# Kernel tuning notes

Measured on AMD Instinct MI355X. Metric: run time of the kernel, lower is better.

The kernel has to match this reference:

```python
import jax, jax.numpy as jnp
import numpy as np

B, IN, OUT, LUT_SIZE = 32, 8192, 16384, 256


def setup_inputs() -> dict:
    key = jax.random.key(0)
    k1, k2, k3 = jax.random.split(key, 3)
    x = jax.random.normal(k1, (B, IN), dtype=jnp.float32)
    # int8 weight codes, stored as indices in [0, 256) into the dequant LUT
    weight_idx = jax.random.randint(k2, (OUT, IN), 0, LUT_SIZE, dtype=jnp.int32)
    # symmetric uniform dequant levels: code c -> (c - 128) * scale
    scale = jnp.float32(0.05 / 128.0)
    lut = (jnp.arange(LUT_SIZE, dtype=jnp.float32) - 128.0) * scale  # [256]
    bias = jax.random.normal(k3, (OUT,), dtype=jnp.float32) * 0.02
    return {"x": x, "lut": lut, "bias": bias, "weight_idx": weight_idx}


def reference(x, lut, bias, weight_idx):
    # LUT dequantization: gather fp32 weight values from the 256-entry table
    W = lut[weight_idx]                      # [OUT, IN] fp32
    # y = x @ W^T + b   (einsum: b=batch tokens, i=in_features, o=out_features)
    return jnp.einsum("bi,oi->bo", x, W) + bias  # [B, OUT]
```

## Files before the change

kernel.cpp:

```cpp
#include <hip/hip_runtime.h>

#define IN_F   8192
#define OUT_F  16384
#define BATCH  32
#define NWAVE  4
#define KSLICE (IN_F / NWAVE)

typedef __attribute__((ext_vector_type(8))) short  bf16x8;
typedef __attribute__((ext_vector_type(4))) float  f32x4;

__device__ __forceinline__ unsigned f2bf(float f) {
    unsigned u = __builtin_bit_cast(unsigned, f);
    return (u + 0x7fffu + ((u >> 16) & 1u)) >> 16;
}

__device__ __forceinline__ unsigned pk_i2bf(int a, int b) {
    unsigned fa = __builtin_bit_cast(unsigned, (float)a);
    unsigned fb = __builtin_bit_cast(unsigned, (float)b);
#if __has_builtin(__builtin_amdgcn_perm)
    return __builtin_amdgcn_perm(fb, fa, 0x07060302u);
#else
    return (fa >> 16) | (fb & 0xffff0000u);
#endif
}

__global__ __launch_bounds__(256) void prep_kernel(
        const float* __restrict__ x, const float* __restrict__ lut,
        unsigned short* __restrict__ xbf, float* __restrict__ sumx) {
    const int b = blockIdx.x;
    const int t = threadIdx.x;
    const float s = lut[129];
    const float4* xr = (const float4*)(x + b * IN_F);
    ushort4* xo = (ushort4*)(xbf + b * IN_F);
    float acc = 0.f;
    #pragma unroll
    for (int i = 0; i < IN_F / 4 / 256; ++i) {
        float4 v = xr[t + i * 256];
        acc += v.x + v.y + v.z + v.w;
        ushort4 o;
        o.x = (unsigned short)f2bf(v.x * s);
        o.y = (unsigned short)f2bf(v.y * s);
        o.z = (unsigned short)f2bf(v.z * s);
        o.w = (unsigned short)f2bf(v.w * s);
        xo[t + i * 256] = o;
    }
    __shared__ float red[256];
    red[t] = acc;
    __syncthreads();
    for (int off = 128; off > 0; off >>= 1) {
        if (t < off) red[t] += red[t + off];
        __syncthreads();
    }
    if (t == 0) sumx[b] = red[0];
}

__global__ __launch_bounds__(256) void init_kernel(
        const float* __restrict__ bias, const float* __restrict__ lut,
        const float* __restrict__ sumx, float* __restrict__ out) {
    int i = blockIdx.x * 256 + threadIdx.x;
    int b = i >> 12;
    float corr = lut[0] * sumx[b];
    const float4* b4 = (const float4*)bias;
    float4 v = b4[i & 4095];
    v.x += corr; v.y += corr; v.z += corr; v.w += corr;
    ((float4*)out)[i] = v;
}

__global__ __launch_bounds__(256, 4) void gemm_kernel(
        const unsigned short* __restrict__ xbf,
        const int* __restrict__ widx,
        float* __restrict__ out) {
    const int tid   = threadIdx.x;
    const int wave  = tid >> 6;
    const int lane  = tid & 63;
    const int col16 = lane & 15;
    const int quad  = lane >> 4;
    const int ntile = blockIdx.x;
    const int n     = ntile * 16 + col16;
    const int k0    = wave * KSLICE + quad * 8;

    const int* wp = widx + (long)n * IN_F + k0;
    const unsigned short* xp0 = xbf + col16 * IN_F + k0;
    const unsigned short* xp1 = xp0 + 16 * IN_F;

    f32x4 acc0 = {0.f, 0.f, 0.f, 0.f};
    f32x4 acc1 = {0.f, 0.f, 0.f, 0.f};

    #pragma unroll 2
    for (int kk = 0; kk < KSLICE; kk += 64) {
        int4 wA0 = *(const int4*)(wp + kk);
        int4 wA1 = *(const int4*)(wp + kk + 4);
        int4 wB0 = *(const int4*)(wp + kk + 32);
        int4 wB1 = *(const int4*)(wp + kk + 36);
        bf16x8 xa0 = *(const bf16x8*)(xp0 + kk);
        bf16x8 xa1 = *(const bf16x8*)(xp1 + kk);
        bf16x8 xb0 = *(const bf16x8*)(xp0 + kk + 32);
        bf16x8 xb1 = *(const bf16x8*)(xp1 + kk + 32);

        union { unsigned u[4]; bf16x8 v; } bA, bB;
        bA.u[0] = pk_i2bf(wA0.x, wA0.y);
        bA.u[1] = pk_i2bf(wA0.z, wA0.w);
        bA.u[2] = pk_i2bf(wA1.x, wA1.y);
        bA.u[3] = pk_i2bf(wA1.z, wA1.w);
        bB.u[0] = pk_i2bf(wB0.x, wB0.y);
        bB.u[1] = pk_i2bf(wB0.z, wB0.w);
        bB.u[2] = pk_i2bf(wB1.x, wB1.y);
        bB.u[3] = pk_i2bf(wB1.z, wB1.w);

        acc0 = __builtin_amdgcn_mfma_f32_16x16x32_bf16(xa0, bA.v, acc0, 0, 0, 0);
        acc1 = __builtin_amdgcn_mfma_f32_16x16x32_bf16(xa1, bA.v, acc1, 0, 0, 0);
        acc0 = __builtin_amdgcn_mfma_f32_16x16x32_bf16(xb0, bB.v, acc0, 0, 0, 0);
        acc1 = __builtin_amdgcn_mfma_f32_16x16x32_bf16(xb1, bB.v, acc1, 0, 0, 0);
    }

    const int row = quad * 4;
    float* op = out + (long)ntile * 16 + col16;
    #pragma unroll
    for (int r = 0; r < 4; ++r) {
        unsafeAtomicAdd(op + (long)(row + r) * OUT_F,      acc0[r]);
        unsafeAtomicAdd(op + (long)(row + r + 16) * OUT_F, acc1[r]);
    }
}

extern "C" void kernel_launch(void* const* d_in, const int* in_sizes, int n_in,
                              void* d_out, int out_size, void* d_ws, size_t ws_size,
                              hipStream_t stream) {
    const float* x    = (const float*)d_in[0];
    const float* lut  = (const float*)d_in[1];
    const float* bias = (const float*)d_in[2];
    const int*   widx = (const int*)d_in[3];
    float* out = (float*)d_out;

    unsigned short* xbf = (unsigned short*)d_ws;
    float* sumx = (float*)((char*)d_ws + BATCH * IN_F * 2);

    prep_kernel<<<BATCH, 256, 0, stream>>>(x, lut, xbf, sumx);
    init_kernel<<<(BATCH * OUT_F / 4) / 256, 256, 0, stream>>>(bias, lut, sumx, out);
    gemm_kernel<<<OUT_F / 16, 256, 0, stream>>>(xbf, widx, out);
}
```

Baseline: 714.5 us.

## Fuse bias init into GEMM with LDS split-K reduction and 8 waves

Removes the separate init kernel and replaces the global atomic adds with an in-block shared-memory reduction across eight K-slice waves, then writes bias plus zero-point correction directly. The block size doubles to 512 threads, and the inner loop is restructured to software-prefetch the next 32-wide chunk of weights and activations. This cuts one kernel launch, a full output write/read pass and the atomic traffic, at the cost of an LDS buffer, a block barrier and more registers per thread for the prefetch.

```diff
diff --git a/kernel.cpp b/kernel.cpp
--- a/kernel.cpp
+++ b/kernel.cpp
@@ -3,7 +3,7 @@
 #define IN_F   8192
 #define OUT_F  16384
 #define BATCH  32
-#define NWAVE  4
+#define NWAVE  8
 #define KSLICE (IN_F / NWAVE)
 
 typedef __attribute__((ext_vector_type(8))) short  bf16x8;
@@ -54,22 +54,15 @@
     if (t == 0) sumx[b] = red[0];
 }
 
-__global__ __launch_bounds__(256) void init_kernel(
-        const float* __restrict__ bias, const float* __restrict__ lut,
-        const float* __restrict__ sumx, float* __restrict__ out) {
-    int i = blockIdx.x * 256 + threadIdx.x;
-    int b = i >> 12;
-    float corr = lut[0] * sumx[b];
-    const float4* b4 = (const float4*)bias;
-    float4 v = b4[i & 4095];
-    v.x += corr; v.y += corr; v.z += corr; v.w += corr;
-    ((float4*)out)[i] = v;
-}
-
-__global__ __launch_bounds__(256, 4) void gemm_kernel(
+__global__ __launch_bounds__(512, 6) void gemm_kernel(
         const unsigned short* __restrict__ xbf,
         const int* __restrict__ widx,
+        const float* __restrict__ bias,
+        const float* __restrict__ lut,
+        const float* __restrict__ sumx,
         float* __restrict__ out) {
+    __shared__ float part[NWAVE * 512];
+
     const int tid   = threadIdx.x;
     const int wave  = tid >> 6;
     const int lane  = tid & 63;
@@ -86,39 +79,52 @@
     f32x4 acc0 = {0.f, 0.f, 0.f, 0.f};
     f32x4 acc1 = {0.f, 0.f, 0.f, 0.f};
 
+    int4   c0 = *(const int4*)wp;
+    int4   c1 = *(const int4*)(wp + 4);
+    bf16x8 a0 = *(const bf16x8*)xp0;
+    bf16x8 a1 = *(const bf16x8*)xp1;
+
     #pragma unroll 2
-    for (int kk = 0; kk < KSLICE; kk += 64) {
-        int4 wA0 = *(const int4*)(wp + kk);
-        int4 wA1 = *(const int4*)(wp + kk + 4);
-        int4 wB0 = *(const int4*)(wp + kk + 32);
-        int4 wB1 = *(const int4*)(wp + kk + 36);
-        bf16x8 xa0 = *(const bf16x8*)(xp0 + kk);
-        bf16x8 xa1 = *(const bf16x8*)(xp1 + kk);
-        bf16x8 xb0 = *(const bf16x8*)(xp0 + kk + 32);
-        bf16x8 xb1 = *(const bf16x8*)(xp1 + kk + 32);
+    for (int kk = 32; kk < KSLICE; kk += 32) {
+        int4   p0 = *(const int4*)(wp + kk);
+        int4   p1 = *(const int4*)(wp + kk + 4);
+        bf16x8 q0 = *(const bf16x8*)(xp0 + kk);
+        bf16x8 q1 = *(const bf16x8*)(xp1 + kk);
 
-        union { unsigned u[4]; bf16x8 v; } bA, bB;
-        bA.u[0] = pk_i2bf(wA0.x, wA0.y);
-        bA.u[1] = pk_i2bf(wA0.z, wA0.w);
-        bA.u[2] = pk_i2bf(wA1.x, wA1.y);
-        bA.u[3] = pk_i2bf(wA1.z, wA1.w);
-        bB.u[0] = pk_i2bf(wB0.x, wB0.y);
-        bB.u[1] = pk_i2bf(wB0.z, wB0.w);
-        bB.u[2] = pk_i2bf(wB1.x, wB1.y);
-        bB.u[3] = pk_i2bf(wB1.z, wB1.w);
+        union { unsigned u[4]; bf16x8 v; } bB;
+        bB.u[0] = pk_i2bf(c0.x, c0.y);
+        bB.u[1] = pk_i2bf(c0.z, c0.w);
+        bB.u[2] = pk_i2bf(c1.x, c1.y);
+        bB.u[3] = pk_i2bf(c1.z, c1.w);
+        acc0 = __builtin_amdgcn_mfma_f32_16x16x32_bf16(a0, bB.v, acc0, 0, 0, 0);
+        acc1 = __builtin_amdgcn_mfma_f32_16x16x32_bf16(a1, bB.v, acc1, 0, 0, 0);
 
-        acc0 = __builtin_amdgcn_mfma_f32_16x16x32_bf16(xa0, bA.v, acc0, 0, 0, 0);
-        acc1 = __builtin_amdgcn_mfma_f32_16x16x32_bf16(xa1, bA.v, acc1, 0, 0, 0);
-        acc0 = __builtin_amdgcn_mfma_f32_16x16x32_bf16(xb0, bB.v, acc0, 0, 0, 0);
-        acc1 = __builtin_amdgcn_mfma_f32_16x16x32_bf16(xb1, bB.v, acc1, 0, 0, 0);
+        c0 = p0; c1 = p1; a0 = q0; a1 = q1;
+    }
+    {
+        union { unsigned u[4]; bf16x8 v; } bB;
+        bB.u[0] = pk_i2bf(c0.x, c0.y);
+        bB.u[1] = pk_i2bf(c0.z, c0.w);
+        bB.u[2] = pk_i2bf(c1.x, c1.y);
+        bB.u[3] = pk_i2bf(c1.z, c1.w);
+        acc0 = __builtin_amdgcn_mfma_f32_16x16x32_bf16(a0, bB.v, acc0, 0, 0, 0);
+        acc1 = __builtin_amdgcn_mfma_f32_16x16x32_bf16(a1, bB.v, acc1, 0, 0, 0);
     }
 
-    const int row = quad * 4;
-    float* op = out + (long)ntile * 16 + col16;
     #pragma unroll
     for (int r = 0; r < 4; ++r) {
-        unsafeAtomicAdd(op + (long)(row + r) * OUT_F,      acc0[r]);
-        unsafeAtomicAdd(op + (long)(row + r + 16) * OUT_F, acc1[r]);
+        part[wave * 512 + (quad * 4 + r) * 16 + col16]        = acc0[r];
+        part[wave * 512 + (quad * 4 + r + 16) * 16 + col16]   = acc1[r];
+    }
+    __syncthreads();
+
+    {
+        const int m = tid >> 4, nn = tid & 15;
+        float ssum = 0.f;
+        #pragma unroll
+        for (int w = 0; w < NWAVE; ++w) ssum += part[w * 512 + tid];
+        float o = bias[ntile * 16 + nn] + lut[0] * sumx[m] + ssum;
+        out[(long)m * OUT_F + ntile * 16 + nn] = o;
     }
 }
 
@@ -135,6 +141,5 @@
     float* sumx = (float*)((char*)d_ws + BATCH * IN_F * 2);
 
     prep_kernel<<<BATCH, 256, 0, stream>>>(x, lut, xbf, sumx);
-    init_kernel<<<(BATCH * OUT_F / 4) / 256, 256, 0, stream>>>(bias, lut, sumx, out);
-    gemm_kernel<<<OUT_F / 16, 256, 0, stream>>>(xbf, widx, out);
+    gemm_kernel<<<OUT_F / 16, 512, 0, stream>>>(xbf, widx, bias, lut, sumx, out);
 }
```

Measured after the change: 741.3 us. +3.8%, slower.
